# Performance work log

Measured on AMD Instinct MI355X. Metric: run time of the kernel, lower is better.

The kernel has to match this reference:

```python
import jax, jax.numpy as jnp
import numpy as np

H = 2048        # hidden_size
TWO_H = 4096    # encoder output dim (2*H)
SEQ = 8192      # encoder sequence length


def setup_inputs() -> dict:
    key = jax.random.key(0)
    k1, k2, k3, k4 = jax.random.split(key, 4)
    hidden = jax.random.normal(k1, (H,), dtype=jnp.float32)
    encoder_outputs = jax.random.normal(k2, (SEQ, TWO_H), dtype=jnp.float32)
    # nn.Linear(2H, H): weight [H, 2H], bias [H]
    W = jax.random.normal(k3, (H, TWO_H), dtype=jnp.float32) * (1.0 / np.sqrt(TWO_H))
    b = jax.random.normal(k4, (H,), dtype=jnp.float32) * 0.01
    return {"hidden": hidden, "encoder_outputs": encoder_outputs, "W": W, "b": b}


def reference(hidden, encoder_outputs, W, b):
    # energy_i = W @ enc_i + b ; score_i = hidden . energy_i  -> batched over seq
    # [S, 2H] @ [2H, H] -> [S, H]
    energy = jnp.einsum("se,he->sh", encoder_outputs, W) + b
    scores = energy @ hidden                      # [S]
    attn = jax.nn.softmax(scores, axis=0)         # softmax over seq
    return attn[None, None, :]                    # [1, 1, S]
```

## Files before the change

### kernel.cpp

```cpp
#include <hip/hip_runtime.h>
#include <math.h>

#define HDIM   2048
#define TWOH   4096
#define SEQLEN 8192
#define ROW_CHUNKS 32

__global__ __launch_bounds__(256) void wtv_partial_kernel(
    const float* __restrict__ W, const float* __restrict__ hidden,
    float* __restrict__ partial)
{
    const int e  = blockIdx.x * 256 + threadIdx.x;
    const int h0 = blockIdx.y * 64;
    float acc = 0.0f;
#pragma unroll
    for (int i = 0; i < 64; ++i) {
        const int h = h0 + i;
        acc = fmaf(W[(size_t)h * TWOH + e], hidden[h], acc);
    }
    partial[blockIdx.y * TWOH + e] = acc;
}

__global__ __launch_bounds__(256) void wtv_reduce_kernel(
    const float* __restrict__ partial, float* __restrict__ v)
{
    const int e = blockIdx.x * 256 + threadIdx.x;
    float acc = 0.0f;
#pragma unroll
    for (int p = 0; p < ROW_CHUNKS; ++p)
        acc += partial[p * TWOH + e];
    v[e] = acc;
}

__global__ __launch_bounds__(256) void scores_kernel(
    const float* __restrict__ enc, const float* __restrict__ v,
    float* __restrict__ scores)
{
    __shared__ float4 vs[TWOH / 4];
    const float4* v4 = reinterpret_cast<const float4*>(v);
    for (int i = threadIdx.x; i < TWOH / 4; i += 256)
        vs[i] = v4[i];
    __syncthreads();

    const int wave = threadIdx.x >> 6;
    const int lane = threadIdx.x & 63;
    const int r    = blockIdx.x * 4 + wave;

    const float4* e4 = reinterpret_cast<const float4*>(enc) + (size_t)r * (TWOH / 4);
    float acc = 0.0f;
#pragma unroll
    for (int i = 0; i < 16; ++i) {
        const float4 a = e4[i * 64 + lane];
        const float4 b = vs[i * 64 + lane];
        acc += a.x * b.x + a.y * b.y + a.z * b.z + a.w * b.w;
    }
#pragma unroll
    for (int off = 32; off > 0; off >>= 1)
        acc += __shfl_down(acc, off, 64);
    if (lane == 0)
        scores[r] = acc;
}

__global__ __launch_bounds__(1024) void softmax_kernel(
    const float* __restrict__ scores, float* __restrict__ out)
{
    __shared__ float red[16];
    const int t    = threadIdx.x;
    const int wave = t >> 6;
    const int lane = t & 63;

    float x[8];
    float m = -INFINITY;
#pragma unroll
    for (int i = 0; i < 8; ++i) {
        x[i] = scores[t + i * 1024];
        m = fmaxf(m, x[i]);
    }
#pragma unroll
    for (int off = 32; off > 0; off >>= 1)
        m = fmaxf(m, __shfl_down(m, off, 64));
    if (lane == 0) red[wave] = m;
    __syncthreads();
    float gmax = red[0];
#pragma unroll
    for (int w = 1; w < 16; ++w) gmax = fmaxf(gmax, red[w]);
    __syncthreads();

    float s = 0.0f;
#pragma unroll
    for (int i = 0; i < 8; ++i) {
        x[i] = expf(x[i] - gmax);
        s += x[i];
    }
#pragma unroll
    for (int off = 32; off > 0; off >>= 1)
        s += __shfl_down(s, off, 64);
    if (lane == 0) red[wave] = s;
    __syncthreads();
    float gsum = 0.0f;
#pragma unroll
    for (int w = 0; w < 16; ++w) gsum += red[w];

    const float inv = 1.0f / gsum;
#pragma unroll
    for (int i = 0; i < 8; ++i)
        out[t + i * 1024] = x[i] * inv;
}

extern "C" void kernel_launch(void* const* d_in, const int* in_sizes, int n_in,
                              void* d_out, int out_size, void* d_ws, size_t ws_size,
                              hipStream_t stream)
{
    const float* hidden = (const float*)d_in[0];
    const float* enc    = (const float*)d_in[1];
    const float* W      = (const float*)d_in[2];

    float* ws      = (float*)d_ws;
    float* partial = ws;
    float* v       = ws + ROW_CHUNKS * TWOH;
    float* scores  = v + TWOH;
    float* out     = (float*)d_out;

    wtv_partial_kernel<<<dim3(16, ROW_CHUNKS), 256, 0, stream>>>(W, hidden, partial);
    wtv_reduce_kernel<<<16, 256, 0, stream>>>(partial, v);
    scores_kernel<<<SEQLEN / 4, 256, 0, stream>>>(enc, v, scores);
    softmax_kernel<<<1, 1024, 0, stream>>>(scores, out);
}
```

Before: 243.8 us.

## Fuse softmax into scores kernel via last-block counter; vectorize W^T·hidden

Merges the softmax into the scores kernel using an atomic counter, so the last block to finish computes the softmax over all scores and one kernel launch is saved. The W^T·hidden partial and reduce kernels now use float4 loads, with 64 row chunks of 32 rows and 4 column blocks. The scores loop keeps two accumulators. The fused softmax runs in a single 256-thread block holding 32 values per thread, which lengthens the serial tail, and the reduce kernel now runs on only 4 blocks and reads 64 partials per element.

```diff
diff --git a/kernel.cpp b/kernel.cpp
--- a/kernel.cpp
+++ b/kernel.cpp
@@ -4,107 +4,126 @@
 #define HDIM   2048
 #define TWOH   4096
 #define SEQLEN 8192
-#define ROW_CHUNKS 32
+#define RCHUNK 32
+#define NCHUNK (HDIM / RCHUNK)
+#define C4     (TWOH / 4)
+
 
 __global__ __launch_bounds__(256) void wtv_partial_kernel(
-    const float* __restrict__ W, const float* __restrict__ hidden,
-    float* __restrict__ partial)
+    const float4* __restrict__ W4, const float* __restrict__ hidden,
+    float4* __restrict__ partial4, int* __restrict__ counter)
 {
-    const int e  = blockIdx.x * 256 + threadIdx.x;
-    const int h0 = blockIdx.y * 64;
-    float acc = 0.0f;
-#pragma unroll
-    for (int i = 0; i < 64; ++i) {
-        const int h = h0 + i;
-        acc = fmaf(W[(size_t)h * TWOH + e], hidden[h], acc);
+    __shared__ float hs[RCHUNK];
+    const int tx = threadIdx.x;
+    const int h0 = blockIdx.y * RCHUNK;
+    if (tx < RCHUNK) hs[tx] = hidden[h0 + tx];
+    __syncthreads();
+
+    const int c = blockIdx.x * 256 + tx;
+    float4 acc = {0.f, 0.f, 0.f, 0.f};
+#pragma unroll 8
+    for (int i = 0; i < RCHUNK; ++i) {
+        const float4 w = W4[(size_t)(h0 + i) * C4 + c];
+        const float  s = hs[i];
+        acc.x = fmaf(w.x, s, acc.x);
+        acc.y = fmaf(w.y, s, acc.y);
+        acc.z = fmaf(w.z, s, acc.z);
+        acc.w = fmaf(w.w, s, acc.w);
     }
-    partial[blockIdx.y * TWOH + e] = acc;
+    partial4[(size_t)blockIdx.y * C4 + c] = acc;
+
+    if (tx == 0 && blockIdx.x == 0 && blockIdx.y == 0) *counter = 0;
 }
 
 __global__ __launch_bounds__(256) void wtv_reduce_kernel(
-    const float* __restrict__ partial, float* __restrict__ v)
+    const float4* __restrict__ partial4, float4* __restrict__ v4)
 {
-    const int e = blockIdx.x * 256 + threadIdx.x;
-    float acc = 0.0f;
+    const int c = blockIdx.x * 256 + threadIdx.x;
+    float4 acc = {0.f, 0.f, 0.f, 0.f};
 #pragma unroll
-    for (int p = 0; p < ROW_CHUNKS; ++p)
-        acc += partial[p * TWOH + e];
-    v[e] = acc;
+    for (int p = 0; p < NCHUNK; ++p) {
+        const float4 t = partial4[(size_t)p * C4 + c];
+        acc.x += t.x; acc.y += t.y; acc.z += t.z; acc.w += t.w;
+    }
+    v4[c] = acc;
 }
 
-__global__ __launch_bounds__(256) void scores_kernel(
-    const float* __restrict__ enc, const float* __restrict__ v,
-    float* __restrict__ scores)
+__global__ __launch_bounds__(256) void scores_softmax_kernel(
+    const float4* __restrict__ enc4, const float4* __restrict__ v4,
+    float* __restrict__ scores, int* __restrict__ counter,
+    float* __restrict__ out)
 {
-    __shared__ float4 vs[TWOH / 4];
-    const float4* v4 = reinterpret_cast<const float4*>(v);
-    for (int i = threadIdx.x; i < TWOH / 4; i += 256)
-        vs[i] = v4[i];
+    __shared__ float4 vs[C4];
+    const int tid = threadIdx.x;
+    for (int i = tid; i < C4; i += 256) vs[i] = v4[i];
     __syncthreads();
 
-    const int wave = threadIdx.x >> 6;
-    const int lane = threadIdx.x & 63;
+    const int wave = tid >> 6;
+    const int lane = tid & 63;
     const int r    = blockIdx.x * 4 + wave;
 
-    const float4* e4 = reinterpret_cast<const float4*>(enc) + (size_t)r * (TWOH / 4);
-    float acc = 0.0f;
+    const float4* e4 = enc4 + (size_t)r * C4;
+    float a0 = 0.f, a1 = 0.f;
 #pragma unroll
-    for (int i = 0; i < 16; ++i) {
-        const float4 a = e4[i * 64 + lane];
-        const float4 b = vs[i * 64 + lane];
-        acc += a.x * b.x + a.y * b.y + a.z * b.z + a.w * b.w;
+    for (int i = 0; i < 16; i += 2) {
+        const float4 x0 = e4[i * 64 + lane];
+        const float4 b0 = vs[i * 64 + lane];
+        const float4 x1 = e4[(i + 1) * 64 + lane];
+        const float4 b1 = vs[(i + 1) * 64 + lane];
+        a0 += x0.x * b0.x + x0.y * b0.y + x0.z * b0.z + x0.w * b0.w;
+        a1 += x1.x * b1.x + x1.y * b1.y + x1.z * b1.z + x1.w * b1.w;
     }
+    float acc = a0 + a1;
 #pragma unroll
     for (int off = 32; off > 0; off >>= 1)
         acc += __shfl_down(acc, off, 64);
-    if (lane == 0)
+    if (lane == 0) {
         scores[r] = acc;
-}
+        __threadfence();
+    }
+    __syncthreads();
 
-__global__ __launch_bounds__(1024) void softmax_kernel(
-    const float* __restrict__ scores, float* __restrict__ out)
-{
-    __shared__ float red[16];
-    const int t    = threadIdx.x;
-    const int wave = t >> 6;
-    const int lane = t & 63;
+    __shared__ int amLast;
+    if (tid == 0) {
+        amLast = (atomicAdd(counter, 1) == (int)gridDim.x - 1);
+        if (amLast) __threadfence();
+    }
+    __syncthreads();
+    if (!amLast) return;
 
-    float x[8];
+    float x[32];
     float m = -INFINITY;
 #pragma unroll
-    for (int i = 0; i < 8; ++i) {
-        x[i] = scores[t + i * 1024];
+    for (int i = 0; i < 32; ++i) {
+        x[i] = scores[tid + i * 256];
         m = fmaxf(m, x[i]);
     }
 #pragma unroll
     for (int off = 32; off > 0; off >>= 1)
-        m = fmaxf(m, __shfl_down(m, off, 64));
+        m = fmaxf(m, __shfl_xor(m, off, 64));
+    __shared__ float red[4];
     if (lane == 0) red[wave] = m;
     __syncthreads();
-    float gmax = red[0];
+    m = fmaxf(fmaxf(red[0], red[1]), fmaxf(red[2], red[3]));
+
+    float s = 0.f;
 #pragma unroll
-    for (int w = 1; w < 16; ++w) gmax = fmaxf(gmax, red[w]);
-    __syncthreads();
-
-    float s = 0.0f;
-#pragma unroll
-    for (int i = 0; i < 8; ++i) {
-        x[i] = expf(x[i] - gmax);
+    for (int i = 0; i < 32; ++i) {
+        x[i] = expf(x[i] - m);
         s += x[i];
     }
 #pragma unroll
     for (int off = 32; off > 0; off >>= 1)
-        s += __shfl_down(s, off, 64);
+        s += __shfl_xor(s, off, 64);
+    __syncthreads();
     if (lane == 0) red[wave] = s;
     __syncthreads();
-    float gsum = 0.0f;
+    s = red[0] + red[1] + red[2] + red[3];
+
+    const float inv = 1.f / s;
 #pragma unroll
-    for (int w = 0; w < 16; ++w) gsum += red[w];
-
-    const float inv = 1.0f / gsum;
-#pragma unroll
-    for (int i = 0; i < 8; ++i)
-        out[t + i * 1024] = x[i] * inv;
+    for (int i = 0; i < 32; ++i)
+        out[tid + i * 256] = x[i] * inv;
 }
 
 extern "C" void kernel_launch(void* const* d_in, const int* in_sizes, int n_in,
@@ -117,12 +136,15 @@
 
     float* ws      = (float*)d_ws;
     float* partial = ws;
-    float* v       = ws + ROW_CHUNKS * TWOH;
+    float* v       = partial + NCHUNK * TWOH;
     float* scores  = v + TWOH;
+    int*   counter = (int*)(scores + SEQLEN);
     float* out     = (float*)d_out;
 
-    wtv_partial_kernel<<<dim3(16, ROW_CHUNKS), 256, 0, stream>>>(W, hidden, partial);
-    wtv_reduce_kernel<<<16, 256, 0, stream>>>(partial, v);
-    scores_kernel<<<SEQLEN / 4, 256, 0, stream>>>(enc, v, scores);
-    softmax_kernel<<<1, 1024, 0, stream>>>(scores, out);
+    wtv_partial_kernel<<<dim3(4, NCHUNK), 256, 0, stream>>>(
+        (const float4*)W, hidden, (float4*)partial, counter);
+    wtv_reduce_kernel<<<4, 256, 0, stream>>>(
+        (const float4*)partial, (float4*)v);
+    scores_softmax_kernel<<<SEQLEN / 4, 256, 0, stream>>>(
+        (const float4*)enc, (const float4*)v, scores, counter, out);
 }
```

New measurement: 559.4 us. 129% more time.
